# Kernel optimization log

Hardware: AMD Instinct MI355X
Metric: run time of the kernel (lower is better)

The kernel has to match this reference:

```python
import jax, jax.numpy as jnp
import numpy as np

DIM = 2048
THRESH = 0.33

def _ternary(w):
    # sign() with dead zone: {-1, 0, +1}; detached from grad (matches torch.no_grad)
    return jax.lax.stop_gradient(jnp.where(jnp.abs(w) < THRESH, 0.0, jnp.sign(w)))

def _bitlinear(x, w, b):
    # F.linear(x, ternary_w, bias): x @ ternary_w.T + b
    return jnp.einsum('bsd,od->bso', x, _ternary(w)) + b

def setup_inputs() -> dict:
    key = jax.random.key(0)
    ks = jax.random.split(key, 6)
    B, S, D = 8, 2048, DIM
    x = jax.random.normal(ks[0], (B, S, D), dtype=jnp.float32)
    h_prev = jax.random.normal(ks[1], (B, S, D), dtype=jnp.float32)
    # BitLinear reset_parameters: uniform(-1, 1); bias zeros
    wf = jax.random.uniform(ks[2], (D, D), minval=-1.0, maxval=1.0, dtype=jnp.float32)
    wc = jax.random.uniform(ks[3], (D, D), minval=-1.0, maxval=1.0, dtype=jnp.float32)
    wg = jax.random.uniform(ks[4], (D, D), minval=-1.0, maxval=1.0, dtype=jnp.float32)
    wo = jax.random.uniform(ks[5], (D, D), minval=-1.0, maxval=1.0, dtype=jnp.float32)
    bf = jnp.zeros((D,), dtype=jnp.float32)
    bc = jnp.zeros((D,), dtype=jnp.float32)
    bg = jnp.zeros((D,), dtype=jnp.float32)
    bo = jnp.zeros((D,), dtype=jnp.float32)
    return {"x": x, "h_prev": h_prev, "wf": wf, "bf": bf, "wc": wc, "bc": bc,
            "wg": wg, "bg": bg, "wo": wo, "bo": bo}

def reference(x, h_prev, wf, bf, wc, bc, wg, bg, wo, bo):
    f = jax.nn.sigmoid(_bitlinear(x, wf, bf))
    c = jax.nn.silu(_bitlinear(x, wc, bc))
    h = f * h_prev + (1.0 - f) * c
    g = jax.nn.sigmoid(_bitlinear(x, wg, bg))
    o = _bitlinear(g * h, wo, bo)
    return (o, h)
```

## Files before the change

kernel.cpp:

```cpp
#include <hip/hip_runtime.h>
#include <hip/hip_bf16.h>
#include <cstdint>

#define DIM   2048
#define MROWS 16384
#define NH    64

typedef __bf16 bf16x8 __attribute__((ext_vector_type(8)));
typedef float  f32x4  __attribute__((ext_vector_type(4)));
typedef unsigned short u16;
typedef unsigned int   u32;

#define BARRIER() asm volatile("s_barrier" ::: "memory")
#define WAITVM(N) asm volatile("s_waitcnt vmcnt(" #N ")" ::: "memory")


__device__ __forceinline__ u16 ternary_bits(float w) {
    u32 u = __float_as_uint(w);
    u16 s = (u16)((u >> 16) & 0x8000u);
    return (__builtin_fabsf(w) < 0.33f) ? (u16)0 : (u16)(0x3F80u | s);
}

__device__ __forceinline__ u16 f2bf_rne(float f) {
    u32 u = __float_as_uint(f);
    u32 r = (u + 0x7FFFu + ((u >> 16) & 1u)) >> 16;
    return (u16)r;
}

__device__ __forceinline__ void gload16(const void* g, void* l) {
    __builtin_amdgcn_global_load_lds(
        (const __attribute__((address_space(1))) void*)g,
        (__attribute__((address_space(3))) void*)l,
        16, 0, 0);
}


__global__ void prep_weights(const float* __restrict__ wf, const float* __restrict__ wc,
                             const float* __restrict__ wg, const float* __restrict__ wo,
                             u16* __restrict__ out) {
    const float* srcs[4] = {wf, wc, wg, wo};
    const float* src = srcs[blockIdx.y];
    u16* dst = out + (size_t)blockIdx.y * (DIM * DIM);
    int e = (blockIdx.x * 256 + threadIdx.x) * 8;
    float4 v0 = *(const float4*)(src + e);
    float4 v1 = *(const float4*)(src + e + 4);
    ushort4 o0, o1;
    o0.x = ternary_bits(v0.x); o0.y = ternary_bits(v0.y);
    o0.z = ternary_bits(v0.z); o0.w = ternary_bits(v0.w);
    o1.x = ternary_bits(v1.x); o1.y = ternary_bits(v1.y);
    o1.z = ternary_bits(v1.z); o1.w = ternary_bits(v1.w);
    *(ushort4*)(dst + e)     = o0;
    *(ushort4*)(dst + e + 4) = o1;
}

__global__ void cast_x(const float* __restrict__ x, u16* __restrict__ xb) {
    size_t e = ((size_t)blockIdx.x * 256 + threadIdx.x) * 8;
    float4 v0 = *(const float4*)(x + e);
    float4 v1 = *(const float4*)(x + e + 4);
    ushort4 o0, o1;
    o0.x = f2bf_rne(v0.x); o0.y = f2bf_rne(v0.y);
    o0.z = f2bf_rne(v0.z); o0.w = f2bf_rne(v0.w);
    o1.x = f2bf_rne(v1.x); o1.y = f2bf_rne(v1.y);
    o1.z = f2bf_rne(v1.z); o1.w = f2bf_rne(v1.w);
    *(ushort4*)(xb + e)     = o0;
    *(ushort4*)(xb + e + 4) = o1;
}


__global__ __launch_bounds__(512) void gemm1(
    const u16* __restrict__ xb,
    const u16* __restrict__ wt,
    const float* __restrict__ bfv_, const float* __restrict__ bcv_, const float* __restrict__ bgv_,
    const float* __restrict__ hprev,
    float* __restrict__ hout,
    u16* __restrict__ gh)
{
    __shared__ __align__(16) u16 lds[3 * 20480];

    const int tid  = threadIdx.x;
    const int lane = tid & 63;
    const int wave = tid >> 6;
    const int wr   = wave >> 2;
    const int wcq  = wave & 3;

    const int bid  = blockIdx.x;
    const int swz  = (bid & 7) * 128 + (bid >> 3);
    const int brow = (swz & 63) * 256;
    const int bcol = (swz >> 6) * 128;

    const int srow = tid >> 2;
    const int gc4  = (tid & 3) ^ ((tid >> 3) & 3);
    const int ldst = tid * 8;

    const int fr  = lane & 15;
    const int hi  = lane >> 4;
    const int csw = (hi ^ ((fr >> 1) & 3)) * 8;

    f32x4 acc0[3][8] = {};
    f32x4 acc1[3][8] = {};

    const u16* aSrc0 = xb + (size_t)(brow + srow) * DIM;
    const u16* aSrc1 = xb + (size_t)(brow + 128 + srow) * DIM;
    const u16* bSrcB = wt + (size_t)(bcol + srow) * DIM;
    const size_t WST = (size_t)DIM * DIM;

    auto issueA = [&](int so, int k0) {
        gload16(aSrc0 + k0 + gc4 * 8, (u16*)&lds[so + ldst]);
        gload16(aSrc1 + k0 + gc4 * 8, (u16*)&lds[so + 4096 + ldst]);
    };
    auto issueB = [&](int so, int k0, int g) {
        gload16(bSrcB + (size_t)g * WST + k0 + gc4 * 8,
                (u16*)&lds[so + 8192 + g * 4096 + ldst]);
    };

    auto rdA = [&](int so, bf16x8 (&a)[8]) {
        #pragma unroll
        for (int mi = 0; mi < 8; ++mi)
            a[mi] = *(const bf16x8*)(&lds[so + (wr * 128 + mi * 16 + fr) * 32 + csw]);
    };
    auto rdB = [&](int so, int ni, bf16x8 (&b)[3]) {
        #pragma unroll
        for (int g = 0; g < 3; ++g)
            b[g] = *(const bf16x8*)(&lds[so + 8192 + g * 4096 + (wcq * 32 + ni * 16 + fr) * 32 + csw]);
    };
    auto domfma = [&](bf16x8 (&a)[8], bf16x8 (&b)[3], f32x4 (&c)[3][8]) {
        __builtin_amdgcn_s_setprio(1);
        #pragma unroll
        for (int g = 0; g < 3; ++g)
            #pragma unroll
            for (int mi = 0; mi < 8; ++mi)
                c[g][mi] = __builtin_amdgcn_mfma_f32_16x16x32_bf16(a[mi], b[g], c[g][mi], 0, 0, 0);
        __builtin_amdgcn_s_setprio(0);
    };

    int so0 = 0, so1 = 20480, so2 = 40960;

    issueA(so0, 0); issueB(so0, 0, 0); issueB(so0, 0, 1); issueB(so0, 0, 2);
    issueA(so1, 32); issueB(so1, 32, 0); issueB(so1, 32, 1); issueB(so1, 32, 2);
    WAITVM(5);
    BARRIER();

    bf16x8 a[8], b[3];
    #pragma unroll 1
    for (int h = 0; h < NH - 2; ++h) {
        const int kn = (h + 2) * 32;
        rdA(so0, a); rdB(so0, 0, b);
        issueA(so2, kn); issueB(so2, kn, 0);
        BARRIER();
        domfma(a, b, acc0);
        BARRIER();
        rdB(so0, 1, b);
        issueB(so2, kn, 1); issueB(so2, kn, 2);
        WAITVM(5);
        BARRIER();
        domfma(a, b, acc1);
        BARRIER();
        int t = so0; so0 = so1; so1 = so2; so2 = t;
    }
    rdA(so0, a); rdB(so0, 0, b);
    BARRIER(); domfma(a, b, acc0); BARRIER();
    rdB(so0, 1, b);
    WAITVM(0);
    BARRIER(); domfma(a, b, acc1); BARRIER();
    { int t = so0; so0 = so1; so1 = so2; so2 = t; }
    rdA(so0, a); rdB(so0, 0, b);
    domfma(a, b, acc0);
    rdB(so0, 1, b);
    domfma(a, b, acc1);

    auto epi = [&](int ni, f32x4 (&c)[3][8]) {
        const int col = bcol + wcq * 32 + ni * 16 + fr;
        const float bfv = bfv_[col], bcv = bcv_[col], bgv = bgv_[col];
        #pragma unroll
        for (int mi = 0; mi < 8; ++mi) {
            #pragma unroll
            for (int j = 0; j < 4; ++j) {
                const int row = brow + wr * 128 + mi * 16 + hi * 4 + j;
                const size_t idx = (size_t)row * DIM + col;
                float pf = c[0][mi][j] + bfv;
                float pc = c[1][mi][j] + bcv;
                float pg = c[2][mi][j] + bgv;
                float f  = 1.f / (1.f + __expf(-pf));
                float cc = pc / (1.f + __expf(-pc));
                float g  = 1.f / (1.f + __expf(-pg));
                float hh = f * hprev[idx] + (1.f - f) * cc;
                hout[idx] = hh;
                gh[idx] = f2bf_rne(g * hh);
            }
        }
    };
    epi(0, acc0);
    epi(1, acc1);
}


__global__ __launch_bounds__(512) void gemm2(
    const u16* __restrict__ gh,
    const u16* __restrict__ wot,
    const float* __restrict__ bov_,
    float* __restrict__ oout)
{
    __shared__ __align__(16) u16 lds[3 * 16384];

    const int tid  = threadIdx.x;
    const int lane = tid & 63;
    const int wave = tid >> 6;
    const int wr   = wave >> 2;
    const int wcq  = wave & 3;

    const int bid  = blockIdx.x;
    const int swz  = (bid & 7) * 64 + (bid >> 3);
    const int brow = (swz & 63) * 256;
    const int bcol = (swz >> 6) * 256;

    const int srow = tid >> 2;
    const int gc4  = (tid & 3) ^ ((tid >> 3) & 3);
    const int ldst = tid * 8;

    const int fr  = lane & 15;
    const int hi  = lane >> 4;
    const int csw = (hi ^ ((fr >> 1) & 3)) * 8;

    f32x4 accL[8][2] = {};
    f32x4 accH[8][2] = {};

    const u16* aSrc0 = gh  + (size_t)(brow + srow) * DIM;
    const u16* aSrc1 = gh  + (size_t)(brow + 128 + srow) * DIM;
    const u16* bSrc0 = wot + (size_t)(bcol + srow) * DIM;
    const u16* bSrc1 = wot + (size_t)(bcol + 128 + srow) * DIM;

    auto issueA = [&](int so, int k0) {
        gload16(aSrc0 + k0 + gc4 * 8, (u16*)&lds[so + ldst]);
        gload16(aSrc1 + k0 + gc4 * 8, (u16*)&lds[so + 4096 + ldst]);
    };
    auto issueB = [&](int so, int k0) {
        gload16(bSrc0 + k0 + gc4 * 8, (u16*)&lds[so + 8192 + ldst]);
        gload16(bSrc1 + k0 + gc4 * 8, (u16*)&lds[so + 12288 + ldst]);
    };

    auto rdA = [&](int so, bf16x8 (&a)[8]) {
        #pragma unroll
        for (int mi = 0; mi < 8; ++mi)
            a[mi] = *(const bf16x8*)(&lds[so + (wr * 128 + mi * 16 + fr) * 32 + csw]);
    };
    auto rdB2 = [&](int so, int nbase, bf16x8 (&b)[2]) {
        #pragma unroll
        for (int jn = 0; jn < 2; ++jn)
            b[jn] = *(const bf16x8*)(&lds[so + 8192 + (wcq * 64 + (nbase + jn) * 16 + fr) * 32 + csw]);
    };
    auto domfma2 = [&](bf16x8 (&a)[8], bf16x8 (&b)[2], f32x4 (&c)[8][2]) {
        __builtin_amdgcn_s_setprio(1);
        #pragma unroll
        for (int jn = 0; jn < 2; ++jn)
            #pragma unroll
            for (int mi = 0; mi < 8; ++mi)
                c[mi][jn] = __builtin_amdgcn_mfma_f32_16x16x32_bf16(a[mi], b[jn], c[mi][jn], 0, 0, 0);
        __builtin_amdgcn_s_setprio(0);
    };

    int so0 = 0, so1 = 16384, so2 = 32768;

    issueA(so0, 0); issueB(so0, 0);
    issueA(so1, 32); issueB(so1, 32);
    WAITVM(4);
    BARRIER();

    bf16x8 a[8], b[2];
    #pragma unroll 1
    for (int h = 0; h < NH - 2; ++h) {
        const int kn = (h + 2) * 32;
        rdA(so0, a); rdB2(so0, 0, b);
        issueA(so2, kn);
        BARRIER();
        domfma2(a, b, accL);
        BARRIER();
        rdB2(so0, 2, b);
        issueB(so2, kn);
        WAITVM(4);
        BARRIER();
        domfma2(a, b, accH);
        BARRIER();
        int t = so0; so0 = so1; so1 = so2; so2 = t;
    }
    rdA(so0, a); rdB2(so0, 0, b);
    BARRIER(); domfma2(a, b, accL); BARRIER();
    rdB2(so0, 2, b);
    WAITVM(0);
    BARRIER(); domfma2(a, b, accH); BARRIER();
    { int t = so0; so0 = so1; so1 = so2; so2 = t; }
    rdA(so0, a); rdB2(so0, 0, b);
    domfma2(a, b, accL);
    rdB2(so0, 2, b);
    domfma2(a, b, accH);

    auto epi2 = [&](int nbase, f32x4 (&c)[8][2]) {
        #pragma unroll
        for (int jn = 0; jn < 2; ++jn) {
            const int col = bcol + wcq * 64 + (nbase + jn) * 16 + fr;
            const float bov = bov_[col];
            #pragma unroll
            for (int mi = 0; mi < 8; ++mi)
                #pragma unroll
                for (int j = 0; j < 4; ++j)
                    oout[(size_t)(brow + wr * 128 + mi * 16 + hi * 4 + j) * DIM + col] = c[mi][jn][j] + bov;
        }
    };
    epi2(0, accL);
    epi2(2, accH);
}

extern "C" void kernel_launch(void* const* d_in, const int* in_sizes, int n_in,
                              void* d_out, int out_size, void* d_ws, size_t ws_size,
                              hipStream_t stream) {
    const float* x  = (const float*)d_in[0];
    const float* hp = (const float*)d_in[1];
    const float* wf = (const float*)d_in[2];
    const float* bf = (const float*)d_in[3];
    const float* wc = (const float*)d_in[4];
    const float* bc = (const float*)d_in[5];
    const float* wg = (const float*)d_in[6];
    const float* bg = (const float*)d_in[7];
    const float* wo = (const float*)d_in[8];
    const float* bo = (const float*)d_in[9];

    float* o_out = (float*)d_out;
    float* h_out = o_out + (size_t)MROWS * DIM;

    u16* w_t  = (u16*)d_ws;
    u16* x_bf = (u16*)((char*)d_ws + 33554432);
    u16* gh   = (u16*)((char*)d_ws + 100663296);

    prep_weights<<<dim3(2048, 4), 256, 0, stream>>>(wf, wc, wg, wo, w_t);
    cast_x<<<dim3(16384), 256, 0, stream>>>(x, x_bf);
    gemm1<<<dim3(1024), 512, 0, stream>>>(x_bf, w_t, bf, bc, bg, hp, h_out, gh);
    gemm2<<<dim3(512), 512, 0, stream>>>(gh, w_t + 3 * (size_t)DIM * DIM, bo, o_out);
}
```

Measured before the change: 819.5 us.

## Halve gemm1 row tile and switch to four-slot single-barrier pipeline

The fused gate GEMM now uses a 128-row by 128-column (times three weights) block tile instead of 256 rows, which halves accumulator registers and doubles the grid to 2048 blocks. The LDS pipeline becomes four slots of 16K elements, with loads issued three stages ahead and a single wait/barrier pair per k-step instead of two half-steps. The aim is higher occupancy, less register pressure and a deeper prefetch. In exchange, each A/B load is reused across fewer output elements, so L2 and global traffic per FLOP goes up.

```diff
diff --git a/kernel.cpp b/kernel.cpp
--- a/kernel.cpp
+++ b/kernel.cpp
@@ -75,7 +75,7 @@
     float* __restrict__ hout,
     u16* __restrict__ gh)
 {
-    __shared__ __align__(16) u16 lds[3 * 20480];
+    __shared__ __align__(16) u16 lds[4][16384];
 
     const int tid  = threadIdx.x;
     const int lane = tid & 63;
@@ -84,98 +84,95 @@
     const int wcq  = wave & 3;
 
     const int bid  = blockIdx.x;
-    const int swz  = (bid & 7) * 128 + (bid >> 3);
-    const int brow = (swz & 63) * 256;
-    const int bcol = (swz >> 6) * 128;
-
-    const int srow = tid >> 2;
-    const int gc4  = (tid & 3) ^ ((tid >> 3) & 3);
-    const int ldst = tid * 8;
+    const int swz  = (bid & 7) * 256 + (bid >> 3);
+    const int brow = (swz & 127) * 128;
+    const int bcol = (swz >> 7) * 128;
+
+    const int row512 = tid >> 2;
+    const int gc4    = (tid & 3) ^ ((tid >> 3) & 3);
+    const int ldst   = tid * 8;
 
     const int fr  = lane & 15;
     const int hi  = lane >> 4;
     const int csw = (hi ^ ((fr >> 1) & 3)) * 8;
 
-    f32x4 acc0[3][8] = {};
-    f32x4 acc1[3][8] = {};
-
-    const u16* aSrc0 = xb + (size_t)(brow + srow) * DIM;
-    const u16* aSrc1 = xb + (size_t)(brow + 128 + srow) * DIM;
-    const u16* bSrcB = wt + (size_t)(bcol + srow) * DIM;
+    f32x4 acc0[3][4] = {};
+    f32x4 acc1[3][4] = {};
+
+    const u16* aSrc  = xb + (size_t)(brow + row512) * DIM;
+    const u16* bSrc0 = wt + (size_t)(bcol + row512) * DIM;
     const size_t WST = (size_t)DIM * DIM;
 
-    auto issueA = [&](int so, int k0) {
-        gload16(aSrc0 + k0 + gc4 * 8, (u16*)&lds[so + ldst]);
-        gload16(aSrc1 + k0 + gc4 * 8, (u16*)&lds[so + 4096 + ldst]);
-    };
-    auto issueB = [&](int so, int k0, int g) {
-        gload16(bSrcB + (size_t)g * WST + k0 + gc4 * 8,
-                (u16*)&lds[so + 8192 + g * 4096 + ldst]);
-    };
-
-    auto rdA = [&](int so, bf16x8 (&a)[8]) {
-        #pragma unroll
-        for (int mi = 0; mi < 8; ++mi)
-            a[mi] = *(const bf16x8*)(&lds[so + (wr * 128 + mi * 16 + fr) * 32 + csw]);
-    };
-    auto rdB = [&](int so, int ni, bf16x8 (&b)[3]) {
+    auto issueHalf = [&](int slot, int k0) {
+        gload16(aSrc + k0 + gc4 * 8,                (u16*)&lds[slot][ldst]);
+        gload16(bSrc0 + 0 * WST + k0 + gc4 * 8,     (u16*)&lds[slot][4096  + ldst]);
+        gload16(bSrc0 + 1 * WST + k0 + gc4 * 8,     (u16*)&lds[slot][8192  + ldst]);
+        gload16(bSrc0 + 2 * WST + k0 + gc4 * 8,     (u16*)&lds[slot][12288 + ldst]);
+    };
+
+    auto rdFrags = [&](const u16* sl, bf16x8 (&a)[4], bf16x8 (&b0)[3], bf16x8 (&b1)[3]) {
+        #pragma unroll
+        for (int mi = 0; mi < 4; ++mi)
+            a[mi] = *(const bf16x8*)(sl + (wr * 64 + mi * 16 + fr) * 32 + csw);
         #pragma unroll
         for (int g = 0; g < 3; ++g)
-            b[g] = *(const bf16x8*)(&lds[so + 8192 + g * 4096 + (wcq * 32 + ni * 16 + fr) * 32 + csw]);
-    };
-    auto domfma = [&](bf16x8 (&a)[8], bf16x8 (&b)[3], f32x4 (&c)[3][8]) {
+            b0[g] = *(const bf16x8*)(sl + 4096 + g * 4096 + (wcq * 32 + fr) * 32 + csw);
+        #pragma unroll
+        for (int g = 0; g < 3; ++g)
+            b1[g] = *(const bf16x8*)(sl + 4096 + g * 4096 + (wcq * 32 + 16 + fr) * 32 + csw);
+    };
+
+    auto cluster = [&](bf16x8 (&a)[4], bf16x8 (&b0)[3], bf16x8 (&b1)[3]) {
         __builtin_amdgcn_s_setprio(1);
         #pragma unroll
         for (int g = 0; g < 3; ++g)
             #pragma unroll
-            for (int mi = 0; mi < 8; ++mi)
-                c[g][mi] = __builtin_amdgcn_mfma_f32_16x16x32_bf16(a[mi], b[g], c[g][mi], 0, 0, 0);
+            for (int mi = 0; mi < 4; ++mi)
+                acc0[g][mi] = __builtin_amdgcn_mfma_f32_16x16x32_bf16(a[mi], b0[g], acc0[g][mi], 0, 0, 0);
+        #pragma unroll
+        for (int g = 0; g < 3; ++g)
+            #pragma unroll
+            for (int mi = 0; mi < 4; ++mi)
+                acc1[g][mi] = __builtin_amdgcn_mfma_f32_16x16x32_bf16(a[mi], b1[g], acc1[g][mi], 0, 0, 0);
         __builtin_amdgcn_s_setprio(0);
     };
 
-    int so0 = 0, so1 = 20480, so2 = 40960;
-
-    issueA(so0, 0); issueB(so0, 0, 0); issueB(so0, 0, 1); issueB(so0, 0, 2);
-    issueA(so1, 32); issueB(so1, 32, 0); issueB(so1, 32, 1); issueB(so1, 32, 2);
-    WAITVM(5);
-    BARRIER();
-
-    bf16x8 a[8], b[3];
+    issueHalf(0, 0); issueHalf(1, 32); issueHalf(2, 64);
+    WAITVM(8);
+    BARRIER();
+
+    bf16x8 a[4], b0[3], b1[3];
     #pragma unroll 1
-    for (int h = 0; h < NH - 2; ++h) {
-        const int kn = (h + 2) * 32;
-        rdA(so0, a); rdB(so0, 0, b);
-        issueA(so2, kn); issueB(so2, kn, 0);
-        BARRIER();
-        domfma(a, b, acc0);
-        BARRIER();
-        rdB(so0, 1, b);
-        issueB(so2, kn, 1); issueB(so2, kn, 2);
-        WAITVM(5);
-        BARRIER();
-        domfma(a, b, acc1);
-        BARRIER();
-        int t = so0; so0 = so1; so1 = so2; so2 = t;
+    for (int j = 0; j < NH - 3; ++j) {
+        const u16* sl = &lds[j & 3][0];
+        issueHalf((j + 3) & 3, (j + 3) * 32);
+        rdFrags(sl, a, b0, b1);
+        WAITVM(8);
+        BARRIER();
+        cluster(a, b0, b1);
+        BARRIER();
     }
-    rdA(so0, a); rdB(so0, 0, b);
-    BARRIER(); domfma(a, b, acc0); BARRIER();
-    rdB(so0, 1, b);
+    rdFrags(&lds[(NH - 3) & 3][0], a, b0, b1);
+    WAITVM(4);
+    BARRIER();
+    cluster(a, b0, b1);
+    BARRIER();
+    rdFrags(&lds[(NH - 2) & 3][0], a, b0, b1);
     WAITVM(0);
-    BARRIER(); domfma(a, b, acc1); BARRIER();
-    { int t = so0; so0 = so1; so1 = so2; so2 = t; }
-    rdA(so0, a); rdB(so0, 0, b);
-    domfma(a, b, acc0);
-    rdB(so0, 1, b);
-    domfma(a, b, acc1);
-
-    auto epi = [&](int ni, f32x4 (&c)[3][8]) {
+    BARRIER();
+    cluster(a, b0, b1);
+    BARRIER();
+    rdFrags(&lds[(NH - 1) & 3][0], a, b0, b1);
+    cluster(a, b0, b1);
+
+    auto epi = [&](int ni, f32x4 (&c)[3][4]) {
         const int col = bcol + wcq * 32 + ni * 16 + fr;
         const float bfv = bfv_[col], bcv = bcv_[col], bgv = bgv_[col];
         #pragma unroll
-        for (int mi = 0; mi < 8; ++mi) {
+        for (int mi = 0; mi < 4; ++mi) {
             #pragma unroll
             for (int j = 0; j < 4; ++j) {
-                const int row = brow + wr * 128 + mi * 16 + hi * 4 + j;
+                const int row = brow + wr * 64 + mi * 16 + hi * 4 + j;
                 const size_t idx = (size_t)row * DIM + col;
                 float pf = c[0][mi][j] + bfv;
                 float pc = c[1][mi][j] + bcv;
@@ -332,6 +329,6 @@
 
     prep_weights<<<dim3(2048, 4), 256, 0, stream>>>(wf, wc, wg, wo, w_t);
     cast_x<<<dim3(16384), 256, 0, stream>>>(x, x_bf);
-    gemm1<<<dim3(1024), 512, 0, stream>>>(x_bf, w_t, bf, bc, bg, hp, h_out, gh);
+    gemm1<<<dim3(2048), 512, 0, stream>>>(x_bf, w_t, bf, bc, bg, hp, h_out, gh);
     gemm2<<<dim3(512), 512, 0, stream>>>(gh, w_t + 3 * (size_t)DIM * DIM, bo, o_out);
 }
```

After: 722.1 us. 11.9% less time.
